# Optimization experiments

Measured on AMD Instinct MI355X. Metric: run time of the kernel, lower is better.

Reference implementation:

```python
import jax, jax.numpy as jnp
import numpy as np

STATE_DIM = 512
ACTION_FEAT_DIM = 64
HIDDEN = 256


def setup_inputs() -> dict:
    key = jax.random.key(0)
    ks = jax.random.split(key, 8)
    B, K = 256, 1000
    state_embed = jax.random.normal(ks[0], (B, STATE_DIM), dtype=jnp.float32)
    action_feats = jax.random.normal(ks[1], (B, K, ACTION_FEAT_DIM), dtype=jnp.float32)
    s = 0.05
    W1 = jax.random.normal(ks[2], (STATE_DIM + ACTION_FEAT_DIM, HIDDEN), dtype=jnp.float32) * s
    b1 = jnp.zeros((HIDDEN,), dtype=jnp.float32)
    W2 = jax.random.normal(ks[3], (HIDDEN, HIDDEN // 2), dtype=jnp.float32) * s
    b2 = jnp.zeros((HIDDEN // 2,), dtype=jnp.float32)
    W3 = jax.random.normal(ks[4], (HIDDEN // 2, 1), dtype=jnp.float32) * s
    b3 = jnp.zeros((1,), dtype=jnp.float32)
    return {"state_embed": state_embed, "action_feats": action_feats,
            "W1": W1, "b1": b1, "W2": W2, "b2": b2, "W3": W3, "b3": b3}


def reference(state_embed, action_feats, W1, b1, W2, b2, W3, b3):
    # Faithful math: concat([state broadcast to K, action_feats]) -> Linear/ReLU x2 -> Linear(1)
    # Efficient form: split W1 rows so state part is computed once per batch row.
    W1_s = W1[:STATE_DIM]            # [state_dim, hidden]
    W1_a = W1[STATE_DIM:]            # [action_feat_dim, hidden]
    h_state = state_embed @ W1_s     # [B, hidden]
    h = jax.nn.relu(jnp.einsum('bkf,fh->bkh', action_feats, W1_a) + h_state[:, None, :] + b1)
    h = jax.nn.relu(jnp.einsum('bkh,hg->bkg', h, W2) + b2)
    logits = (jnp.einsum('bkg,go->bko', h, W3) + b3)[..., 0]  # [B, K]
    return logits
```

## Files before the change

kernel.cpp:

```cpp
#include <hip/hip_runtime.h>

typedef _Float16 f16;
typedef f16 f16x4 __attribute__((ext_vector_type(4)));
typedef f16 f16x8 __attribute__((ext_vector_type(8)));
typedef float f32x4 __attribute__((ext_vector_type(4)));


#define AF_STRIDE 64
#define H1_STRIDE 256

__global__ __launch_bounds__(256) void prep_kernel(const float* __restrict__ W1,
                                                   const float* __restrict__ W2,
                                                   const float* __restrict__ state,
                                                   const float* __restrict__ b1,
                                                   f16* __restrict__ pw1at,
                                                   f16* __restrict__ pw2,
                                                   float* __restrict__ hstate) {
    __shared__ float srow[512];
    int blk = blockIdx.x;
    int tid = threadIdx.x;
    if (blk < 24) {
        int idx = blk * 256 + tid;
        int F = idx >> 6;
        int L = idx & 63;
        int q = L >> 4, c = L & 15;
        f16x8 v;
        if (F < 32) {
            int mt = F >> 1, kt = F & 1;
            #pragma unroll
            for (int j = 0; j < 8; ++j) {
                int f = kt * 32 + q * 8 + j;
                v[j] = (f16)W1[(size_t)(512 + f) * 256 + mt * 16 + c];
            }
            *(f16x8*)(pw1at + ((size_t)F * 64 + L) * 8) = v;
        } else {
            int F2 = F - 32;
            int nt = F2 >> 3, kt = F2 & 7;
            #pragma unroll
            for (int j = 0; j < 8; ++j) {
                int k = kt * 32 + q * 8 + j;
                v[j] = (f16)W2[(size_t)k * 128 + nt * 16 + c];
            }
            *(f16x8*)(pw2 + ((size_t)F2 * 64 + L) * 8) = v;
        }
    } else {
        int b = blk - 24;
        srow[tid] = state[(size_t)b * 512 + tid];
        srow[tid + 256] = state[(size_t)b * 512 + 256 + tid];
        __syncthreads();
        float a0 = 0.f, a1 = 0.f;
        #pragma unroll 16
        for (int f = 0; f < 512; f += 2) {
            a0 = fmaf(srow[f],     W1[(size_t)f * 256 + tid],       a0);
            a1 = fmaf(srow[f + 1], W1[(size_t)(f + 1) * 256 + tid], a1);
        }
        hstate[(size_t)b * 256 + tid] = a0 + a1 + b1[tid];
    }
}

__global__ __launch_bounds__(256, 4) void fused_kernel(const float* __restrict__ afeat,
                                                       const float* __restrict__ hstate,
                                                       const f16* __restrict__ pw1at,
                                                       const f16* __restrict__ pw2,
                                                       const float* __restrict__ b2,
                                                       const float* __restrict__ W3,
                                                       const float* __restrict__ b3,
                                                       float* __restrict__ out) {
    __shared__ __align__(16) char smem[(64 * AF_STRIDE + 64 * H1_STRIDE) * 2];
    f16* afs = (f16*)smem;
    f16* h1s = (f16*)(smem + 64 * AF_STRIDE * 2);
    float* lds3 = (float*)smem;

    int tid = threadIdx.x;
    int w = tid >> 6;
    int L = tid & 63;
    int q = L >> 4, c = L & 15;
    int r0 = blockIdx.x * 64;

    f16x8 a1f[4][2];
    #pragma unroll
    for (int i = 0; i < 4; ++i)
        #pragma unroll
        for (int kt = 0; kt < 2; ++kt)
            a1f[i][kt] = *(const f16x8*)(pw1at + ((size_t)((4 * w + i) * 2 + kt) * 64 + L) * 8);

    #pragma unroll
    for (int i = 0; i < 2; ++i) {
        int id = i * 256 + tid;
        int row = id >> 3, c32 = id & 7;
        const float* p = afeat + (size_t)(r0 + row) * 64 + c32 * 8;
        f32x4 lo = *(const f32x4*)p;
        f32x4 hi = *(const f32x4*)(p + 4);
        f16x8 v;
        v[0] = (f16)lo[0]; v[1] = (f16)lo[1]; v[2] = (f16)lo[2]; v[3] = (f16)lo[3];
        v[4] = (f16)hi[0]; v[5] = (f16)hi[1]; v[6] = (f16)hi[2]; v[7] = (f16)hi[3];
        *(f16x8*)(afs + row * AF_STRIDE + ((c32 * 8) ^ ((row & 7) << 3))) = v;
    }

    int b0i = r0 / 1000;
    int boundary = (b0i + 1) * 1000;
    int b1i = b0i < 255 ? b0i + 1 : 255;

    f32x4 hsva[4], hsvb[4];
    #pragma unroll
    for (int i = 0; i < 4; ++i) {
        int hbase = (4 * w + i) * 16 + q * 4;
        hsva[i] = *(const f32x4*)(hstate + (size_t)b0i * 256 + hbase);
        hsvb[i] = *(const f32x4*)(hstate + (size_t)b1i * 256 + hbase);
    }

    float b3v = b3[0];
    __syncthreads();

    int sx = (c & 7) << 3;

    f16x8 bf[4][2];
    #pragma unroll
    for (int nt = 0; nt < 4; ++nt)
        #pragma unroll
        for (int kt = 0; kt < 2; ++kt)
            bf[nt][kt] = *(const f16x8*)(afs + (nt * 16 + c) * AF_STRIDE + ((kt * 32 + q * 8) ^ sx));

    #pragma unroll
    for (int i = 0; i < 4; ++i) {
        f32x4 acc[4];
        #pragma unroll
        for (int nt = 0; nt < 4; ++nt) {
            acc[nt] = (f32x4){0.f, 0.f, 0.f, 0.f};
            #pragma unroll
            for (int kt = 0; kt < 2; ++kt)
                acc[nt] = __builtin_amdgcn_mfma_f32_16x16x32_f16(
                    a1f[i][kt], bf[nt][kt], acc[nt], 0, 0, 0);
        }
        int hbase = (4 * w + i) * 16 + q * 4;
        #pragma unroll
        for (int nt = 0; nt < 4; ++nt) {
            bool sel = (r0 + nt * 16 + c) >= boundary;
            f16x4 hv;
            #pragma unroll
            for (int reg = 0; reg < 4; ++reg) {
                float v = acc[nt][reg] + (sel ? hsvb[i][reg] : hsva[i][reg]);
                v = v > 0.f ? v : 0.f;
                hv[reg] = (f16)v;
            }
            *(f16x4*)(h1s + (nt * 16 + c) * H1_STRIDE + (hbase ^ sx)) = hv;
        }
    }
    __syncthreads();

    f32x4 b2v[2], w3v[2];
    #pragma unroll
    for (int gti = 0; gti < 2; ++gti) {
        int gb = (2 * w + gti) * 16 + q * 4;
        b2v[gti] = *(const f32x4*)(b2 + gb);
        w3v[gti] = *(const f32x4*)(W3 + gb);
    }

    f32x4 acc2[4][2];
    #pragma unroll
    for (int rb = 0; rb < 4; ++rb) {
        acc2[rb][0] = (f32x4){0.f, 0.f, 0.f, 0.f};
        acc2[rb][1] = (f32x4){0.f, 0.f, 0.f, 0.f};
    }

    f16x8 pwf[2][2];
    #pragma unroll
    for (int gti = 0; gti < 2; ++gti)
        pwf[0][gti] = *(const f16x8*)(pw2 + ((size_t)((2 * w + gti) * 8 + 0) * 64 + L) * 8);

    #pragma unroll
    for (int kt = 0; kt < 8; ++kt) {
        if (kt < 7) {
            #pragma unroll
            for (int gti = 0; gti < 2; ++gti)
                pwf[(kt + 1) & 1][gti] =
                    *(const f16x8*)(pw2 + ((size_t)((2 * w + gti) * 8 + kt + 1) * 64 + L) * 8);
        }
        f16x8 a2[4];
        #pragma unroll
        for (int rb = 0; rb < 4; ++rb)
            a2[rb] = *(const f16x8*)(h1s + (rb * 16 + c) * H1_STRIDE + ((kt * 32 + q * 8) ^ sx));
        #pragma unroll
        for (int gti = 0; gti < 2; ++gti)
            #pragma unroll
            for (int rb = 0; rb < 4; ++rb)
                acc2[rb][gti] = __builtin_amdgcn_mfma_f32_16x16x32_f16(
                    pwf[kt & 1][gti], a2[rb], acc2[rb][gti], 0, 0, 0);
    }

    float pa[4];
    #pragma unroll
    for (int rb = 0; rb < 4; ++rb) {
        float s = 0.f;
        #pragma unroll
        for (int gti = 0; gti < 2; ++gti)
            #pragma unroll
            for (int reg = 0; reg < 4; ++reg) {
                float v = acc2[rb][gti][reg] + b2v[gti][reg];
                v = v > 0.f ? v : 0.f;
                s = fmaf(v, w3v[gti][reg], s);
            }
        pa[rb] = s;
    }
    #pragma unroll
    for (int rb = 0; rb < 4; ++rb) {
        pa[rb] += __shfl_xor(pa[rb], 16);
        pa[rb] += __shfl_xor(pa[rb], 32);
    }
    if (L < 16) {
        #pragma unroll
        for (int rb = 0; rb < 4; ++rb)
            lds3[(rb * 16 + L) * 6 + w] = pa[rb];
    }
    __syncthreads();

    if (tid < 64) {
        const float* pm = lds3 + tid * 6;
        out[r0 + tid] = pm[0] + pm[1] + pm[2] + pm[3] + b3v;
    }
}

extern "C" void kernel_launch(void* const* d_in, const int* in_sizes, int n_in,
                              void* d_out, int out_size, void* d_ws, size_t ws_size,
                              hipStream_t stream) {
    const float* state = (const float*)d_in[0];
    const float* afeat = (const float*)d_in[1];
    const float* W1    = (const float*)d_in[2];
    const float* b1    = (const float*)d_in[3];
    const float* W2    = (const float*)d_in[4];
    const float* b2    = (const float*)d_in[5];
    const float* W3    = (const float*)d_in[6];
    const float* b3    = (const float*)d_in[7];
    float* out = (float*)d_out;

    float* hstate = (float*)d_ws;
    f16* pw1at = (f16*)((char*)d_ws + 65536 * sizeof(float));
    f16* pw2   = pw1at + 16384;

    prep_kernel<<<280, 256, 0, stream>>>(W1, W2, state, b1, pw1at, pw2, hstate);
    fused_kernel<<<4000, 256, 0, stream>>>(afeat, hstate, pw1at, pw2, b2, W3, b3, out);
}
```

Before: 133.6 us.

## Reorder global loads, fold bias into MFMA accumulator, double-buffer LDS reads

The action-feature global loads are issued before the weight-fragment and hstate loads, and the fp16 conversion and LDS store are deferred so the load latencies overlap. The hstate bias now initializes the layer-1 MFMA accumulator, and ReLU is applied with a packed fp16 max instead of per-element float adds and compares. Layer-2 LDS reads of h1 are double-buffered against the MFMAs, addressing is precomputed as byte offsets, and s_setprio wraps the MFMA block. Register pressure rises, which may affect occupancy under the 4-waves launch bound.

Result: no change. 133.0 us (-0.4%).

```diff
diff --git a/kernel.cpp b/kernel.cpp
--- a/kernel.cpp
+++ b/kernel.cpp
@@ -77,25 +77,22 @@
     int q = L >> 4, c = L & 15;
     int r0 = blockIdx.x * 64;
 
-    f16x8 a1f[4][2];
-    #pragma unroll
-    for (int i = 0; i < 4; ++i)
-        #pragma unroll
-        for (int kt = 0; kt < 2; ++kt)
-            a1f[i][kt] = *(const f16x8*)(pw1at + ((size_t)((4 * w + i) * 2 + kt) * 64 + L) * 8);
-
+    f32x4 sl[2][2];
     #pragma unroll
     for (int i = 0; i < 2; ++i) {
         int id = i * 256 + tid;
         int row = id >> 3, c32 = id & 7;
         const float* p = afeat + (size_t)(r0 + row) * 64 + c32 * 8;
-        f32x4 lo = *(const f32x4*)p;
-        f32x4 hi = *(const f32x4*)(p + 4);
-        f16x8 v;
-        v[0] = (f16)lo[0]; v[1] = (f16)lo[1]; v[2] = (f16)lo[2]; v[3] = (f16)lo[3];
-        v[4] = (f16)hi[0]; v[5] = (f16)hi[1]; v[6] = (f16)hi[2]; v[7] = (f16)hi[3];
-        *(f16x8*)(afs + row * AF_STRIDE + ((c32 * 8) ^ ((row & 7) << 3))) = v;
-    }
+        sl[i][0] = *(const f32x4*)p;
+        sl[i][1] = *(const f32x4*)(p + 4);
+    }
+
+    f16x8 a1f[4][2];
+    #pragma unroll
+    for (int i = 0; i < 4; ++i)
+        #pragma unroll
+        for (int kt = 0; kt < 2; ++kt)
+            a1f[i][kt] = *(const f16x8*)(pw1at + ((size_t)((4 * w + i) * 2 + kt) * 64 + L) * 8);
 
     int b0i = r0 / 1000;
     int boundary = (b0i + 1) * 1000;
@@ -109,41 +106,52 @@
         hsvb[i] = *(const f32x4*)(hstate + (size_t)b1i * 256 + hbase);
     }
 
-    float b3v = b3[0];
+    #pragma unroll
+    for (int i = 0; i < 2; ++i) {
+        int id = i * 256 + tid;
+        int row = id >> 3, c32 = id & 7;
+        f16x8 v;
+        v[0] = (f16)sl[i][0][0]; v[1] = (f16)sl[i][0][1];
+        v[2] = (f16)sl[i][0][2]; v[3] = (f16)sl[i][0][3];
+        v[4] = (f16)sl[i][1][0]; v[5] = (f16)sl[i][1][1];
+        v[6] = (f16)sl[i][1][2]; v[7] = (f16)sl[i][1][3];
+        *(f16x8*)(afs + row * AF_STRIDE + ((c32 * 8) ^ ((row & 7) << 3))) = v;
+    }
     __syncthreads();
 
     int sx = (c & 7) << 3;
-
+    unsigned bo = ((q * 8) ^ sx) * 2;
+
+    const char* Bp0 = (const char*)afs + c * 128 + bo;
+    const char* Bp1 = (const char*)afs + c * 128 + (bo ^ 64);
     f16x8 bf[4][2];
     #pragma unroll
-    for (int nt = 0; nt < 4; ++nt)
-        #pragma unroll
-        for (int kt = 0; kt < 2; ++kt)
-            bf[nt][kt] = *(const f16x8*)(afs + (nt * 16 + c) * AF_STRIDE + ((kt * 32 + q * 8) ^ sx));
-
+    for (int nt = 0; nt < 4; ++nt) {
+        bf[nt][0] = *(const f16x8*)(Bp0 + nt * 2048);
+        bf[nt][1] = *(const f16x8*)(Bp1 + nt * 2048);
+    }
+
+    const f16x4 zf = {(f16)0.f, (f16)0.f, (f16)0.f, (f16)0.f};
     #pragma unroll
     for (int i = 0; i < 4; ++i) {
         f32x4 acc[4];
         #pragma unroll
         for (int nt = 0; nt < 4; ++nt) {
-            acc[nt] = (f32x4){0.f, 0.f, 0.f, 0.f};
+            bool sel = (r0 + nt * 16 + c) >= boundary;
+            acc[nt] = sel ? hsvb[i] : hsva[i];
             #pragma unroll
             for (int kt = 0; kt < 2; ++kt)
                 acc[nt] = __builtin_amdgcn_mfma_f32_16x16x32_f16(
                     a1f[i][kt], bf[nt][kt], acc[nt], 0, 0, 0);
         }
-        int hbase = (4 * w + i) * 16 + q * 4;
+        char* wp = (char*)h1s + c * 512 + ((((4 * w + i) * 16 + q * 4) ^ sx) * 2);
         #pragma unroll
         for (int nt = 0; nt < 4; ++nt) {
-            bool sel = (r0 + nt * 16 + c) >= boundary;
             f16x4 hv;
-            #pragma unroll
-            for (int reg = 0; reg < 4; ++reg) {
-                float v = acc[nt][reg] + (sel ? hsvb[i][reg] : hsva[i][reg]);
-                v = v > 0.f ? v : 0.f;
-                hv[reg] = (f16)v;
-            }
-            *(f16x4*)(h1s + (nt * 16 + c) * H1_STRIDE + (hbase ^ sx)) = hv;
+            hv[0] = (f16)acc[nt][0]; hv[1] = (f16)acc[nt][1];
+            hv[2] = (f16)acc[nt][2]; hv[3] = (f16)acc[nt][3];
+            hv = __builtin_elementwise_max(hv, zf);
+            *(f16x4*)(wp + nt * 8192) = hv;
         }
     }
     __syncthreads();
@@ -155,6 +163,10 @@
         b2v[gti] = *(const f32x4*)(b2 + gb);
         w3v[gti] = *(const f32x4*)(W3 + gb);
     }
+    float b3v = b3[0];
+
+    const char* Ap0 = (const char*)h1s + c * 512 + bo;
+    const char* Ap1 = (const char*)h1s + c * 512 + (bo ^ 64);
 
     f32x4 acc2[4][2];
     #pragma unroll
@@ -163,29 +175,35 @@
         acc2[rb][1] = (f32x4){0.f, 0.f, 0.f, 0.f};
     }
 
-    f16x8 pwf[2][2];
+    f16x8 a2[2][4], pwf[2][2];
+    #pragma unroll
+    for (int rb = 0; rb < 4; ++rb)
+        a2[0][rb] = *(const f16x8*)(Ap0 + rb * 8192);
     #pragma unroll
     for (int gti = 0; gti < 2; ++gti)
-        pwf[0][gti] = *(const f16x8*)(pw2 + ((size_t)((2 * w + gti) * 8 + 0) * 64 + L) * 8);
+        pwf[0][gti] = *(const f16x8*)(pw2 + ((size_t)((2 * w + gti) * 8) * 64 + L) * 8);
 
     #pragma unroll
     for (int kt = 0; kt < 8; ++kt) {
         if (kt < 7) {
+            const char* Apn = ((kt + 1) & 1) ? Ap1 : Ap0;
+            #pragma unroll
+            for (int rb = 0; rb < 4; ++rb)
+                a2[(kt + 1) & 1][rb] =
+                    *(const f16x8*)(Apn + ((kt + 1) >> 1) * 128 + rb * 8192);
             #pragma unroll
             for (int gti = 0; gti < 2; ++gti)
                 pwf[(kt + 1) & 1][gti] =
                     *(const f16x8*)(pw2 + ((size_t)((2 * w + gti) * 8 + kt + 1) * 64 + L) * 8);
         }
-        f16x8 a2[4];
-        #pragma unroll
-        for (int rb = 0; rb < 4; ++rb)
-            a2[rb] = *(const f16x8*)(h1s + (rb * 16 + c) * H1_STRIDE + ((kt * 32 + q * 8) ^ sx));
+        __builtin_amdgcn_s_setprio(1);
         #pragma unroll
         for (int gti = 0; gti < 2; ++gti)
             #pragma unroll
             for (int rb = 0; rb < 4; ++rb)
                 acc2[rb][gti] = __builtin_amdgcn_mfma_f32_16x16x32_f16(
-                    pwf[kt & 1][gti], a2[rb], acc2[rb][gti], 0, 0, 0);
+                    pwf[kt & 1][gti], a2[kt & 1][rb], acc2[rb][gti], 0, 0, 0);
+        __builtin_amdgcn_s_setprio(0);
     }
 
     float pa[4];
```
